# Optimization experiments

Hardware: AMD Instinct MI355X
Metric: run time of the kernel (lower is better)

## Reference

```python
import jax, jax.numpy as jnp
import numpy as np

N_NODES = 50000
N_EDGES = 800000
IN_DIM = 256
EDGE_DIM = 64
EMBED = 128
HEADS = 8
HEAD_DIM = EMBED // HEADS


def mish(x):
    return x * jnp.tanh(jax.nn.softplus(x))


def setup_inputs() -> dict:
    key = jax.random.key(0)
    ks = jax.random.split(key, 9)
    return {
        "node_features": jax.random.normal(ks[0], (N_NODES, IN_DIM), jnp.float32),
        "edge_features": jax.random.normal(ks[1], (N_EDGES, EDGE_DIM), jnp.float32),
        "W_kernel": jax.random.normal(ks[2], (IN_DIM, EMBED), jnp.float32) * (1.0 / np.sqrt(IN_DIM)),
        "W_bias": jax.random.normal(ks[3], (EMBED,), jnp.float32) * 0.01,
        "We_kernel": jax.random.normal(ks[4], (EDGE_DIM, EMBED), jnp.float32) * (1.0 / np.sqrt(EDGE_DIM)),
        "We_bias": jax.random.normal(ks[5], (EMBED,), jnp.float32) * 0.01,
        "a": jax.random.normal(ks[6], (HEADS, HEAD_DIM), jnp.float32) * (1.0 / np.sqrt(HEAD_DIM)),
        "senders": jax.random.randint(ks[7], (N_EDGES,), 0, N_NODES, jnp.int32),
        "receivers": jax.random.randint(ks[8], (N_EDGES,), 0, N_NODES, jnp.int32),
    }


def reference(node_features, edge_features, W_kernel, W_bias, We_kernel, We_bias, a, senders, receivers):
    num_nodes = node_features.shape[-2]
    # shared projection (share_weights=True): h_send == h_recv
    h = node_features @ W_kernel + W_bias                      # [N, D]
    e_send = h[senders]                                        # [E, D] gather
    e_recv = h[receivers]                                      # [E, D] gather
    e_attn = e_send + e_recv + (edge_features @ We_kernel + We_bias)
    e_attn = mish(e_attn).reshape(-1, HEADS, HEAD_DIM)         # [E, H, Dh]
    logits = jnp.einsum('ehd,hd->eh', e_attn, a)               # [E, H]
    # segment softmax over receiver groups
    seg_max = jax.ops.segment_max(logits, receivers, num_segments=num_nodes)  # [N, H]
    ex = jnp.exp(logits - seg_max[receivers])
    denom = jax.ops.segment_sum(ex, receivers, num_segments=num_nodes)
    weights = ex / denom[receivers]                            # [E, H]
    # weighted scatter-sum of sender features
    msg = (weights[..., None] * e_send.reshape(-1, HEADS, HEAD_DIM)).reshape(-1, EMBED)
    nodes = jax.ops.segment_sum(msg, receivers, num_segments=num_nodes)       # [N, D]
    return nodes
```

## Files before the change

kernel.cpp:

```cpp
#include <hip/hip_runtime.h>
#include <math.h>

#define NN 50000
#define NE 800000
#define IND 256
#define ED 64
#define EMB 128
#define NH 8
#define HD 16

typedef short bf16x8 __attribute__((ext_vector_type(8)));
typedef float f32x4 __attribute__((ext_vector_type(4)));

#define NPT  (NN / 16)
#define NPB  ((NPT + 3) / 4)
#define NE4  (NE / 4)
#define NHB  ((NE4 + 255) / 256)
#define NB   ((NN + 511) / 512)

__device__ __forceinline__ unsigned short rne16(float f) {
    unsigned u = __float_as_uint(f);
    unsigned r = u + 0x7FFFu + ((u >> 16) & 1u);
    return (unsigned short)(r >> 16);
}

__device__ __forceinline__ float bf2f(unsigned short s) {
    return __uint_as_float(((unsigned)s) << 16);
}

__device__ __forceinline__ float mishf(float v) {
    float t = __expf(fminf(v, 20.f));
    float u = 1.f + t;
    u = u * u;
    return v * (u - 1.f) * __builtin_amdgcn_rcpf(u + 1.f);
}

__global__ __launch_bounds__(256) void k_proj_hist(
    const float* __restrict__ X, const float* __restrict__ W,
    const float* __restrict__ b, short* __restrict__ hbf,
    const int* __restrict__ rcv, int* __restrict__ cnt) {
    if (blockIdx.x >= NPB) {
        int e0 = ((blockIdx.x - NPB) * 256 + threadIdx.x) * 4;
        if (e0 + 3 < NE) {
            int4 r4 = *(const int4*)&rcv[e0];
            atomicAdd(&cnt[r4.x], 1);
            atomicAdd(&cnt[r4.y], 1);
            atomicAdd(&cnt[r4.z], 1);
            atomicAdd(&cnt[r4.w], 1);
        }
        return;
    }
    __shared__ short BHs[IND * EMB];
    for (int idx = threadIdx.x * 4; idx < IND * EMB; idx += 256 * 4) {
        float4 wv = *(const float4*)&W[idx];
        int k = idx >> 7;
        int col = idx & 127;
        int kk8 = k >> 5, qq = (k & 31) >> 3, j = k & 7;
        float wf[4] = {wv.x, wv.y, wv.z, wv.w};
        #pragma unroll
        for (int i = 0; i < 4; ++i) {
            int cc = (col + i) & 7, lc = (col + i) >> 3;
            int lane = (qq << 4) | lc;
            BHs[(((cc << 3) | kk8) * 64 + lane) * 8 + j] = (short)rne16(wf[i]);
        }
    }
    __syncthreads();

    const int l = threadIdx.x & 63;
    const int lanecol = l & 15;
    const int q = l >> 4;
    const int wid = (blockIdx.x << 2) + (threadIdx.x >> 6);
    const int nW = NPB << 2;

    float4 bv0 = *(const float4*)&b[lanecol * 8];
    float4 bv1 = *(const float4*)&b[lanecol * 8 + 4];
    float wb[8] = {bv0.x, bv0.y, bv0.z, bv0.w, bv1.x, bv1.y, bv1.z, bv1.w};

    for (int tIdx = wid; tIdx < NPT; tIdx += nW) {
        const int n0 = tIdx * 16;
        f32x4 acc[8];
        #pragma unroll
        for (int c = 0; c < 8; ++c) acc[c] = (f32x4){0.f, 0.f, 0.f, 0.f};
        #pragma unroll
        for (int kk8 = 0; kk8 < 8; ++kk8) {
            const float* ar = X + (size_t)(n0 + lanecol) * IND + kk8 * 32 + q * 8;
            float4 a0 = *(const float4*)ar;
            float4 a1 = *(const float4*)(ar + 4);
            float faf[8] = {a0.x, a0.y, a0.z, a0.w, a1.x, a1.y, a1.z, a1.w};
            bf16x8 ahi;
            #pragma unroll
            for (int j = 0; j < 8; ++j) ahi[j] = (short)rne16(faf[j]);
            #pragma unroll
            for (int c = 0; c < 8; ++c) {
                bf16x8 bh = *(bf16x8*)&BHs[(((c << 3) | kk8) * 64 + l) * 8];
                acc[c] = __builtin_amdgcn_mfma_f32_16x16x32_bf16(ahi, bh, acc[c], 0, 0, 0);
            }
        }
        #pragma unroll
        for (int r = 0; r < 4; ++r) {
            const int node = n0 + (q << 2) + r;
            bf16x8 ov;
            #pragma unroll
            for (int c = 0; c < 8; ++c) ov[c] = (short)rne16(acc[c][r] + wb[c]);
            *(bf16x8*)(hbf + (size_t)node * EMB + lanecol * 8) = ov;
        }
    }
}

__global__ __launch_bounds__(512) void k_part(const int* __restrict__ cnt,
                                              int* __restrict__ rowptr,
                                              int* __restrict__ part) {
    __shared__ int sm[512];
    const int t = threadIdx.x;
    const int idx = blockIdx.x * 512 + t;
    int v = (idx < NN) ? cnt[idx] : 0;
    sm[t] = v;
    __syncthreads();
    #pragma unroll
    for (int off = 1; off < 512; off <<= 1) {
        int y = (t >= off) ? sm[t - off] : 0;
        __syncthreads();
        sm[t] += y;
        __syncthreads();
    }
    if (idx < NN) rowptr[idx] = sm[t] - v;
    if (t == 511) part[blockIdx.x] = sm[511];
}

__global__ __launch_bounds__(512) void k_fix2(const int* __restrict__ part,
                                              int* __restrict__ rowptr,
                                              int* __restrict__ cursor) {
    __shared__ int sm[128];
    const int t = threadIdx.x;
    if (t < 128) sm[t] = (t < NB) ? part[t] : 0;
    __syncthreads();
    #pragma unroll
    for (int off = 1; off < 128; off <<= 1) {
        int y = 0;
        if (t < 128 && t >= off) y = sm[t - off];
        __syncthreads();
        if (t < 128) sm[t] += y;
        __syncthreads();
    }
    const int boff = (blockIdx.x > 0) ? sm[blockIdx.x - 1] : 0;
    const int idx = blockIdx.x * 512 + t;
    if (idx < NN) {
        int r = rowptr[idx] + boff;
        rowptr[idx] = r;
        cursor[idx] = r;
    }
    if (blockIdx.x == 0 && t == 0) rowptr[NN] = NE;
}

__global__ __launch_bounds__(256) void k_bucket(
    const int* __restrict__ snd, const int* __restrict__ rcv,
    int* __restrict__ cursor, int2* __restrict__ rec) {
    int e0 = (blockIdx.x * 256 + threadIdx.x) * 4;
    if (e0 + 3 < NE) {
        int4 s4 = *(const int4*)&snd[e0];
        int4 r4 = *(const int4*)&rcv[e0];
        int p0 = atomicAdd(&cursor[r4.x], 1);
        int p1 = atomicAdd(&cursor[r4.y], 1);
        int p2 = atomicAdd(&cursor[r4.z], 1);
        int p3 = atomicAdd(&cursor[r4.w], 1);
        rec[p0] = make_int2(e0,     s4.x | (r4.x << 16));
        rec[p1] = make_int2(e0 + 1, s4.y | (r4.y << 16));
        rec[p2] = make_int2(e0 + 2, s4.z | (r4.z << 16));
        rec[p3] = make_int2(e0 + 3, s4.w | (r4.w << 16));
    }
}

__global__ __launch_bounds__(256) void k_edge_attn(
    const float* __restrict__ EF, const float* __restrict__ We,
    const float* __restrict__ Web, const float* __restrict__ Av,
    const short* __restrict__ hbf, const int2* __restrict__ rec,
    unsigned short* __restrict__ exbf) {
    __shared__ short BHs[ED * EMB];
    __shared__ float2 WA[144];
    for (int idx = threadIdx.x * 4; idx < ED * EMB; idx += 256 * 4) {
        float4 wv = *(const float4*)&We[idx];
        int k = idx >> 7;
        int col = idx & 127;
        int kk = k >> 5, qq = (k & 31) >> 3, j = k & 7;
        float wf[4] = {wv.x, wv.y, wv.z, wv.w};
        #pragma unroll
        for (int i = 0; i < 4; ++i) {
            int cc = (col + i) & 7, lc = (col + i) >> 3;
            int lane = (qq << 4) | lc;
            BHs[(((cc << 1) | kk) * 64 + lane) * 8 + j] = (short)rne16(wf[i]);
        }
    }
    if (threadIdx.x < 128) {
        int c = threadIdx.x & 7, lc = threadIdx.x >> 3;
        WA[lc * 9 + c] = make_float2(Web[threadIdx.x], Av[threadIdx.x]);
    }
    __syncthreads();

    const int l = threadIdx.x & 63;
    const int lanecol = l & 15;
    const int q = l >> 4;
    const int wid = (blockIdx.x << 2) + (threadIdx.x >> 6);
    const int nW = gridDim.x << 2;
    const int NT = NE / 16;

    for (int tIdx = wid; tIdx < NT; tIdx += nW) {
        int2 rc = rec[(size_t)tIdx * 16 + lanecol];

        bf16x8 hsv0, hrv0, hsv1, hrv1, hsv2, hrv2, hsv3, hrv3;
        {
            unsigned u = (unsigned)__shfl(rc.y, (q << 2) + 0, 16);
            hsv0 = *(const bf16x8*)(hbf + (size_t)(u & 0xFFFFu) * EMB + lanecol * 8);
            hrv0 = *(const bf16x8*)(hbf + (size_t)(u >> 16) * EMB + lanecol * 8);
            u = (unsigned)__shfl(rc.y, (q << 2) + 1, 16);
            hsv1 = *(const bf16x8*)(hbf + (size_t)(u & 0xFFFFu) * EMB + lanecol * 8);
            hrv1 = *(const bf16x8*)(hbf + (size_t)(u >> 16) * EMB + lanecol * 8);
            u = (unsigned)__shfl(rc.y, (q << 2) + 2, 16);
            hsv2 = *(const bf16x8*)(hbf + (size_t)(u & 0xFFFFu) * EMB + lanecol * 8);
            hrv2 = *(const bf16x8*)(hbf + (size_t)(u >> 16) * EMB + lanecol * 8);
            u = (unsigned)__shfl(rc.y, (q << 2) + 3, 16);
            hsv3 = *(const bf16x8*)(hbf + (size_t)(u & 0xFFFFu) * EMB + lanecol * 8);
            hrv3 = *(const bf16x8*)(hbf + (size_t)(u >> 16) * EMB + lanecol * 8);
        }

        const float* ar = EF + (size_t)rc.x * ED + q * 8;
        bf16x8 ahi0, ahi1;
        {
            float4 a0 = *(const float4*)ar;
            float4 a1 = *(const float4*)(ar + 4);
            float4 a2 = *(const float4*)(ar + 32);
            float4 a3 = *(const float4*)(ar + 36);
            ahi0[0] = (short)rne16(a0.x); ahi0[1] = (short)rne16(a0.y);
            ahi0[2] = (short)rne16(a0.z); ahi0[3] = (short)rne16(a0.w);
            ahi0[4] = (short)rne16(a1.x); ahi0[5] = (short)rne16(a1.y);
            ahi0[6] = (short)rne16(a1.z); ahi0[7] = (short)rne16(a1.w);
            ahi1[0] = (short)rne16(a2.x); ahi1[1] = (short)rne16(a2.y);
            ahi1[2] = (short)rne16(a2.z); ahi1[3] = (short)rne16(a2.w);
            ahi1[4] = (short)rne16(a3.x); ahi1[5] = (short)rne16(a3.y);
            ahi1[6] = (short)rne16(a3.z); ahi1[7] = (short)rne16(a3.w);
        }

        float pp[4] = {0.f, 0.f, 0.f, 0.f};
        #pragma unroll
        for (int c = 0; c < 8; ++c) {
            bf16x8 b0 = *(bf16x8*)&BHs[(((c << 1) | 0) * 64 + l) * 8];
            bf16x8 b1 = *(bf16x8*)&BHs[(((c << 1) | 1) * 64 + l) * 8];
            f32x4 a4 = (f32x4){0.f, 0.f, 0.f, 0.f};
            a4 = __builtin_amdgcn_mfma_f32_16x16x32_bf16(ahi0, b0, a4, 0, 0, 0);
            a4 = __builtin_amdgcn_mfma_f32_16x16x32_bf16(ahi1, b1, a4, 0, 0, 0);
            float2 wa = WA[lanecol * 9 + c];
            pp[0] = fmaf(mishf(a4[0] + wa.x + bf2f((unsigned short)hsv0[c]) + bf2f((unsigned short)hrv0[c])), wa.y, pp[0]);
            pp[1] = fmaf(mishf(a4[1] + wa.x + bf2f((unsigned short)hsv1[c]) + bf2f((unsigned short)hrv1[c])), wa.y, pp[1]);
            pp[2] = fmaf(mishf(a4[2] + wa.x + bf2f((unsigned short)hsv2[c]) + bf2f((unsigned short)hrv2[c])), wa.y, pp[2]);
            pp[3] = fmaf(mishf(a4[3] + wa.x + bf2f((unsigned short)hsv3[c]) + bf2f((unsigned short)hrv3[c])), wa.y, pp[3]);
        }

        #pragma unroll
        for (int r = 0; r < 4; ++r) {
            float pr = pp[r];
            pr += __shfl_xor(pr, 1, 16);
            const size_t pos = (size_t)tIdx * 16 + (q << 2) + r;
            if ((lanecol & 1) == 0)
                exbf[pos * NH + (lanecol >> 1)] = rne16(__expf(pr));
        }
    }
}

__global__ __launch_bounds__(256) void k_agg(
    const short* __restrict__ hbf, const int2* __restrict__ rec,
    const unsigned short* __restrict__ exbf, const int* __restrict__ rowptr,
    float* __restrict__ out) {
    const int l = threadIdx.x & 63;
    const int node = blockIdx.x * 4 + (threadIdx.x >> 6);
    if (node >= NN) return;
    const int beg = rowptr[node], end = rowptr[node + 1];
    const int h = l >> 3;
    float a0 = 0.f, a1 = 0.f, den = 0.f;
    int j = beg;
    for (; j + 8 <= end; j += 8) {
        int s[8];
        float ex[8];
        unsigned hv[8];
        #pragma unroll
        for (int i = 0; i < 8; ++i) s[i] = rec[j + i].y & 0xFFFF;
        #pragma unroll
        for (int i = 0; i < 8; ++i) ex[i] = bf2f(exbf[(size_t)(j + i) * NH + h]);
        #pragma unroll
        for (int i = 0; i < 8; ++i)
            hv[i] = *(const unsigned*)(hbf + (size_t)s[i] * EMB + 2 * l);
        #pragma unroll
        for (int i = 0; i < 8; ++i) {
            a0 = fmaf(ex[i], bf2f((unsigned short)(hv[i] & 0xFFFF)), a0);
            a1 = fmaf(ex[i], bf2f((unsigned short)(hv[i] >> 16)), a1);
            den += ex[i];
        }
    }
    for (; j < end; ++j) {
        float ex = bf2f(exbf[(size_t)j * NH + h]);
        unsigned hv = *(const unsigned*)(hbf + (size_t)(rec[j].y & 0xFFFF) * EMB + 2 * l);
        a0 = fmaf(ex, bf2f((unsigned short)(hv & 0xFFFF)), a0);
        a1 = fmaf(ex, bf2f((unsigned short)(hv >> 16)), a1);
        den += ex;
    }
    float rd = (end > beg) ? __builtin_amdgcn_rcpf(den) : 0.f;
    float2 o;
    o.x = a0 * rd;
    o.y = a1 * rd;
    *(float2*)&out[(size_t)node * EMB + 2 * l] = o;
}

extern "C" void kernel_launch(void* const* d_in, const int* in_sizes, int n_in,
                              void* d_out, int out_size, void* d_ws, size_t ws_size,
                              hipStream_t stream) {
    const float* X   = (const float*)d_in[0];
    const float* EF  = (const float*)d_in[1];
    const float* W   = (const float*)d_in[2];
    const float* Wb  = (const float*)d_in[3];
    const float* We  = (const float*)d_in[4];
    const float* Web = (const float*)d_in[5];
    const float* Av  = (const float*)d_in[6];
    const int* snd   = (const int*)d_in[7];
    const int* rcv   = (const int*)d_in[8];
    float* out = (float*)d_out;

    char* ws = (char*)d_ws;
    size_t off = 0;
    unsigned short* exbf = (unsigned short*)(ws + off); off += (size_t)NE * NH * 2;
    int2* rec     = (int2*)(ws + off);  off += (size_t)NE * 8;
    int* rowptr   = (int*)(ws + off);   off += (size_t)(NN + 1) * 4;
    int* cursor   = (int*)(ws + off);   off += (size_t)NN * 4;
    int* part     = (int*)(ws + off);   off += 512;
    short* hbf    = (short*)(ws + off); off += (size_t)NN * EMB * 2;
    int* cnt      = cursor;

    hipMemsetAsync(cnt, 0, (size_t)NN * sizeof(int), stream);
    k_proj_hist<<<NPB + NHB, 256, 0, stream>>>(X, W, Wb, hbf, rcv, cnt);
    k_part<<<NB, 512, 0, stream>>>(cnt, rowptr, part);
    k_fix2<<<NB, 512, 0, stream>>>(part, rowptr, cursor);
    k_bucket<<<NHB, 256, 0, stream>>>(snd, rcv, cursor, rec);
    k_edge_attn<<<2048, 256, 0, stream>>>(EF, We, Web, Av, hbf, rec, exbf);
    k_agg<<<(NN + 3) / 4, 256, 0, stream>>>(hbf, rec, exbf, rowptr, out);
}
```

Measured before the change: 274.0 us.

## Reuse histogram atomic offsets for CSR bucketing and simplify mish

The receiver histogram now records each edge's atomic return value as its slot within the receiver bucket. The bucket kernel then scatters records to rowptr+offset without a second round of atomics on a cursor array. Mish is rewritten with a single exp and rcp using the tanh(softplus) identity, and the aggregation tail gets a 4-wide unrolled step. The cost is an extra 3.2MB offset array written and read, plus a gathered rowptr lookup per edge.

```diff
diff --git a/kernel.cpp b/kernel.cpp
--- a/kernel.cpp
+++ b/kernel.cpp
@@ -29,24 +29,26 @@
 }
 
 __device__ __forceinline__ float mishf(float v) {
-    float t = __expf(fminf(v, 20.f));
-    float u = 1.f + t;
-    u = u * u;
-    return v * (u - 1.f) * __builtin_amdgcn_rcpf(u + 1.f);
+    float w = __expf(v);
+    float p = fmaf(w, w, w + w);
+    float t = fmaf(-2.f, __builtin_amdgcn_rcpf(p + 2.f), 1.f);
+    return v * t;
 }
 
 __global__ __launch_bounds__(256) void k_proj_hist(
     const float* __restrict__ X, const float* __restrict__ W,
     const float* __restrict__ b, short* __restrict__ hbf,
-    const int* __restrict__ rcv, int* __restrict__ cnt) {
+    const int* __restrict__ rcv, int* __restrict__ cnt,
+    int* __restrict__ ord) {
     if (blockIdx.x >= NPB) {
         int e0 = ((blockIdx.x - NPB) * 256 + threadIdx.x) * 4;
         if (e0 + 3 < NE) {
             int4 r4 = *(const int4*)&rcv[e0];
-            atomicAdd(&cnt[r4.x], 1);
-            atomicAdd(&cnt[r4.y], 1);
-            atomicAdd(&cnt[r4.z], 1);
-            atomicAdd(&cnt[r4.w], 1);
+            int o0 = atomicAdd(&cnt[r4.x], 1);
+            int o1 = atomicAdd(&cnt[r4.y], 1);
+            int o2 = atomicAdd(&cnt[r4.z], 1);
+            int o3 = atomicAdd(&cnt[r4.w], 1);
+            *(int4*)&ord[e0] = make_int4(o0, o1, o2, o3);
         }
         return;
     }
@@ -128,8 +130,7 @@
 }
 
 __global__ __launch_bounds__(512) void k_fix2(const int* __restrict__ part,
-                                              int* __restrict__ rowptr,
-                                              int* __restrict__ cursor) {
+                                              int* __restrict__ rowptr) {
     __shared__ int sm[128];
     const int t = threadIdx.x;
     if (t < 128) sm[t] = (t < NB) ? part[t] : 0;
@@ -144,29 +145,23 @@
     }
     const int boff = (blockIdx.x > 0) ? sm[blockIdx.x - 1] : 0;
     const int idx = blockIdx.x * 512 + t;
-    if (idx < NN) {
-        int r = rowptr[idx] + boff;
-        rowptr[idx] = r;
-        cursor[idx] = r;
-    }
+    if (idx < NN) rowptr[idx] += boff;
     if (blockIdx.x == 0 && t == 0) rowptr[NN] = NE;
 }
 
 __global__ __launch_bounds__(256) void k_bucket(
     const int* __restrict__ snd, const int* __restrict__ rcv,
-    int* __restrict__ cursor, int2* __restrict__ rec) {
+    const int* __restrict__ ord, const int* __restrict__ rowptr,
+    int2* __restrict__ rec) {
     int e0 = (blockIdx.x * 256 + threadIdx.x) * 4;
     if (e0 + 3 < NE) {
         int4 s4 = *(const int4*)&snd[e0];
         int4 r4 = *(const int4*)&rcv[e0];
-        int p0 = atomicAdd(&cursor[r4.x], 1);
-        int p1 = atomicAdd(&cursor[r4.y], 1);
-        int p2 = atomicAdd(&cursor[r4.z], 1);
-        int p3 = atomicAdd(&cursor[r4.w], 1);
-        rec[p0] = make_int2(e0,     s4.x | (r4.x << 16));
-        rec[p1] = make_int2(e0 + 1, s4.y | (r4.y << 16));
-        rec[p2] = make_int2(e0 + 2, s4.z | (r4.z << 16));
-        rec[p3] = make_int2(e0 + 3, s4.w | (r4.w << 16));
+        int4 o4 = *(const int4*)&ord[e0];
+        rec[rowptr[r4.x] + o4.x] = make_int2(e0,     s4.x | (r4.x << 16));
+        rec[rowptr[r4.y] + o4.y] = make_int2(e0 + 1, s4.y | (r4.y << 16));
+        rec[rowptr[r4.z] + o4.z] = make_int2(e0 + 2, s4.z | (r4.z << 16));
+        rec[rowptr[r4.w] + o4.w] = make_int2(e0 + 3, s4.w | (r4.w << 16));
     }
 }
 
@@ -294,6 +289,25 @@
             den += ex[i];
         }
     }
+    if (j + 4 <= end) {
+        int s[4];
+        float ex[4];
+        unsigned hv[4];
+        #pragma unroll
+        for (int i = 0; i < 4; ++i) s[i] = rec[j + i].y & 0xFFFF;
+        #pragma unroll
+        for (int i = 0; i < 4; ++i) ex[i] = bf2f(exbf[(size_t)(j + i) * NH + h]);
+        #pragma unroll
+        for (int i = 0; i < 4; ++i)
+            hv[i] = *(const unsigned*)(hbf + (size_t)s[i] * EMB + 2 * l);
+        #pragma unroll
+        for (int i = 0; i < 4; ++i) {
+            a0 = fmaf(ex[i], bf2f((unsigned short)(hv[i] & 0xFFFF)), a0);
+            a1 = fmaf(ex[i], bf2f((unsigned short)(hv[i] >> 16)), a1);
+            den += ex[i];
+        }
+        j += 4;
+    }
     for (; j < end; ++j) {
         float ex = bf2f(exbf[(size_t)j * NH + h]);
         unsigned hv = *(const unsigned*)(hbf + (size_t)(rec[j].y & 0xFFFF) * EMB + 2 * l);
@@ -326,17 +340,17 @@
     size_t off = 0;
     unsigned short* exbf = (unsigned short*)(ws + off); off += (size_t)NE * NH * 2;
     int2* rec     = (int2*)(ws + off);  off += (size_t)NE * 8;
+    int* ord      = (int*)(ws + off);   off += (size_t)NE * 4;
     int* rowptr   = (int*)(ws + off);   off += (size_t)(NN + 1) * 4;
-    int* cursor   = (int*)(ws + off);   off += (size_t)NN * 4;
+    int* cnt      = (int*)(ws + off);   off += (size_t)NN * 4;
     int* part     = (int*)(ws + off);   off += 512;
     short* hbf    = (short*)(ws + off); off += (size_t)NN * EMB * 2;
-    int* cnt      = cursor;
 
     hipMemsetAsync(cnt, 0, (size_t)NN * sizeof(int), stream);
-    k_proj_hist<<<NPB + NHB, 256, 0, stream>>>(X, W, Wb, hbf, rcv, cnt);
+    k_proj_hist<<<NPB + NHB, 256, 0, stream>>>(X, W, Wb, hbf, rcv, cnt, ord);
     k_part<<<NB, 512, 0, stream>>>(cnt, rowptr, part);
-    k_fix2<<<NB, 512, 0, stream>>>(part, rowptr, cursor);
-    k_bucket<<<NHB, 256, 0, stream>>>(snd, rcv, cursor, rec);
+    k_fix2<<<NB, 512, 0, stream>>>(part, rowptr);
+    k_bucket<<<NHB, 256, 0, stream>>>(snd, rcv, ord, rowptr, rec);
     k_edge_attn<<<2048, 256, 0, stream>>>(EF, We, Web, Av, hbf, rec, exbf);
     k_agg<<<(NN + 3) / 4, 256, 0, stream>>>(hbf, rec, exbf, rowptr, out);
 }
```

Measured after the change: 236.6 us. -13.7%, faster.
